# Performance work log

Measured on AMD Instinct MI355X. Metric: run time of the kernel, lower is better.

The kernel has to match this reference:

```python
import jax, jax.numpy as jnp
import numpy as np

FRAME, LATENT, HIDDEN, GATE_H, EXPERTS = 267, 32, 256, 64, 6
BATCH = 4096
IN0 = LATENT + FRAME            # 299: decoder layer-0 input (z, c)
IN1 = LATENT + HIDDEN           # 288: decoder layer-1/2 input (z, h)
OUT = FRAME                     # num_future_predictions * frame_size


def _lin(key, fan_in, fan_out):
    b = np.sqrt(1.0 / fan_in)
    return jax.random.uniform(key, (fan_in, fan_out), jnp.float32, -b, b)


def setup_inputs() -> dict:
    key = jax.random.key(0)
    ks = jax.random.split(key, 16)
    d = {
        "x": jax.random.normal(ks[0], (BATCH, FRAME), jnp.float32),
        "c": jax.random.normal(ks[1], (BATCH, FRAME), jnp.float32),
        "eps": jax.random.normal(ks[2], (BATCH, LATENT), jnp.float32),
        # encoder
        "enc_w1": _lin(ks[3], 2 * FRAME, HIDDEN), "enc_b1": jnp.zeros((HIDDEN,), jnp.float32),
        "enc_w2": _lin(ks[4], FRAME + HIDDEN, HIDDEN), "enc_b2": jnp.zeros((HIDDEN,), jnp.float32),
        "enc_wmu": _lin(ks[5], FRAME + HIDDEN, LATENT), "enc_bmu": jnp.zeros((LATENT,), jnp.float32),
        "enc_wlv": _lin(ks[6], FRAME + HIDDEN, LATENT), "enc_blv": jnp.zeros((LATENT,), jnp.float32),
        # gate MLP
        "g_w0": _lin(ks[7], IN0, GATE_H), "g_b0": jnp.zeros((GATE_H,), jnp.float32),
        "g_w1": _lin(ks[8], GATE_H, GATE_H), "g_b1": jnp.zeros((GATE_H,), jnp.float32),
        "g_w2": _lin(ks[9], GATE_H, EXPERTS), "g_b2": jnp.zeros((EXPERTS,), jnp.float32),
        # expert-mixed decoder layers (kaiming-uniform-ish init, bias 0.01)
        "w0": jax.random.uniform(ks[10], (EXPERTS, IN0, HIDDEN), jnp.float32, -np.sqrt(6.0 / IN0), np.sqrt(6.0 / IN0)),
        "b0": jnp.full((EXPERTS, HIDDEN), 0.01, jnp.float32),
        "w1": jax.random.uniform(ks[11], (EXPERTS, IN1, HIDDEN), jnp.float32, -np.sqrt(6.0 / IN1), np.sqrt(6.0 / IN1)),
        "b1": jnp.full((EXPERTS, HIDDEN), 0.01, jnp.float32),
        "w2": jax.random.uniform(ks[12], (EXPERTS, IN1, OUT), jnp.float32, -np.sqrt(6.0 / IN1), np.sqrt(6.0 / IN1)),
        "b2": jnp.full((EXPERTS, OUT), 0.01, jnp.float32),
    }
    return d


def reference(x, c, eps,
              enc_w1, enc_b1, enc_w2, enc_b2, enc_wmu, enc_bmu, enc_wlv, enc_blv,
              g_w0, g_b0, g_w1, g_b1, g_w2, g_b2,
              w0, b0, w1, b1, w2, b2):
    elu = jax.nn.elu
    # --- encoder ---
    h1 = elu(jnp.concatenate([x, c], axis=1) @ enc_w1 + enc_b1)
    h2 = elu(jnp.concatenate([x, h1], axis=1) @ enc_w2 + enc_b2)
    s = jnp.concatenate([x, h2], axis=1)
    mu = s @ enc_wmu + enc_bmu
    logvar = s @ enc_wlv + enc_blv
    z = mu + eps * jnp.exp(0.5 * logvar)
    # --- gate ---
    zc = jnp.concatenate([z, c], axis=1)
    g = elu(zc @ g_w0 + g_b0)
    g = elu(g @ g_w1 + g_b1)
    coeff = jax.nn.softmax(g @ g_w2 + g_b2, axis=1)  # [N, E]
    # --- soft-MoE decoder: blended-weight per-sample GEMMs ---
    layer = c
    for w, b, act in ((w0, b0, elu), (w1, b1, elu), (w2, b2, None)):
        inp = jnp.concatenate([z, layer], axis=1)  # [N, Din]
        # out[n,o] = sum_e coeff[n,e] * (inp[n,:] @ w[e,:,o]) + coeff[n,:] @ b[:,o]
        out = jnp.einsum('ne,ni,eio->no', coeff, inp, w) + coeff @ b
        layer = act(out) if act is not None else out
    return layer, mu, logvar
```

## Files before the change

kernel.cpp:

```cpp
#include <hip/hip_runtime.h>
#include <hip/hip_bf16.h>
#include <math.h>

#define N_BATCH 4096
#define FRAME   267
#define LATENT  32
#define HIDDEN  256
#define GATE_H  64
#define EXPERTS 6

typedef __hip_bfloat16 bf16;
typedef __bf16  bf16x8 __attribute__((ext_vector_type(8)));
typedef float   f32x4  __attribute__((ext_vector_type(4)));

__device__ __forceinline__ float eluf(float v) { return (v > 0.f) ? v : (expf(v) - 1.f); }

#define MFMA(a, b, p) __builtin_amdgcn_mfma_f32_16x16x32_bf16((a), (b), (p), 0, 0, 0)

struct WEnt { const float* src; bf16* dst; int K, M, Mtot, mOff, Ksteps, Mtiles, cum; };
struct WTab { WEnt e[10]; int total; };

__global__ __launch_bounds__(256) void prep_kernel(
    const float* __restrict__ bmu, const float* __restrict__ blv,
    float* __restrict__ biasCat, WTab tab)
{
    const int tid = threadIdx.x, bid = blockIdx.x;
    if (bid == 0 && tid < 64)
        biasCat[tid] = (tid < 32) ? bmu[tid] : blv[tid - 32];

    __shared__ float tbuf[32][33];
    int i = 0;
    while (i < 9 && bid >= tab.e[i + 1].cum) ++i;
    const WEnt en = tab.e[i];
    const int t = bid - en.cum;
    const int perE = en.Ksteps * en.Mtiles;
    const int e = t / perE;
    const int rr = t - e * perE;
    const int mt = rr / en.Ksteps;
    const int ks = rr - mt * en.Ksteps;
    const int tx = tid & 31, ty = tid >> 5;
    const float* src = en.src + (size_t)e * en.K * en.M;
    #pragma unroll
    for (int i0 = 0; i0 < 32; i0 += 8) {
        const int k = ks * 32 + i0 + ty, m = mt * 32 + tx;
        tbuf[i0 + ty][tx] = (k < en.K && m < en.M) ? src[(size_t)k * en.M + m] : 0.f;
    }
    __syncthreads();
    bf16* dst = en.dst + ((size_t)(e * en.Ksteps + ks) * en.Mtot + en.mOff + mt * 32) * 32;
    #pragma unroll
    for (int i0 = 0; i0 < 32; i0 += 8)
        dst[(size_t)(i0 + ty) * 32 + tx] = __float2bfloat16(tbuf[tx][i0 + ty]);
}

__global__ __launch_bounds__(1024, 2) void fused_kernel(
    const float* __restrict__ x, const float* __restrict__ c,
    const float* __restrict__ eps,
    const bf16* __restrict__ We1, const float* __restrict__ eb1,
    const bf16* __restrict__ We2, const float* __restrict__ eb2,
    const bf16* __restrict__ Wml, const float* __restrict__ biasCat,
    const bf16* __restrict__ Wg0, const float* __restrict__ gb0,
    const bf16* __restrict__ Wg1, const float* __restrict__ gb1,
    const bf16* __restrict__ Wg2, const float* __restrict__ gb2,
    const bf16* __restrict__ W0, const float* __restrict__ b0,
    const bf16* __restrict__ W1, const float* __restrict__ b1,
    const bf16* __restrict__ W2, const float* __restrict__ b2,
    float* __restrict__ out_layer, float* __restrict__ out_mu,
    float* __restrict__ out_lv)
{
    __shared__ bf16  bufA[16 * 552];
    __shared__ bf16  bufB[16 * 552];
    __shared__ float sML[16 * 64];
    __shared__ bf16  sG1[16 * 72];
    __shared__ bf16  sG2[16 * 72];
    __shared__ float sLg[16 * 16];
    __shared__ float sCo[EXPERTS * 16];

    const int tid  = threadIdx.x;
    const int w    = tid >> 6, lane = tid & 63, ml = lane & 15, quad = lane >> 4;
    const int row0 = blockIdx.x * 16;

    {
        const float* xr = x + (size_t)(row0 + w) * FRAME;
        const float* cr = c + (size_t)(row0 + w) * FRAME;
        #pragma unroll
        for (int j = 0; j < 9; ++j) {
            const int col = lane + j * 64;
            if (col < 544) {
                float v = 0.f;
                if (col < FRAME)          v = xr[col];
                else if (col < 2 * FRAME) v = cr[col - FRAME];
                bufA[w * 552 + col] = __float2bfloat16(v);
            }
        }
    }
    __syncthreads();

    {
        const int col = 16 * w + ml;
        f32x4 p = (f32x4){0,0,0,0};
        const bf16* wp = We1 + (size_t)col * 32 + quad * 8;
        #pragma unroll
        for (int ks = 0; ks < 17; ++ks) {
            const bf16x8 a = *(const bf16x8*)(bufA + ml * 552 + ks * 32 + quad * 8);
            p = MFMA(a, *(const bf16x8*)(wp + (size_t)ks * 256 * 32), p);
        }
        const float bv = eb1[col];
        #pragma unroll
        for (int rg = 0; rg < 4; ++rg)
            bufB[(quad * 4 + rg) * 552 + 267 + col] = __float2bfloat16(eluf(p[rg] + bv));
        #pragma unroll
        for (int j = 0; j < 5; ++j) {
            const int cc = lane + j * 64;
            if (cc < 267) bufB[w * 552 + cc] = bufA[w * 552 + cc];
        }
        if (lane < 21) bufB[w * 552 + 523 + lane] = __float2bfloat16(0.f);
    }
    __syncthreads();

    {
        const int col = 16 * w + ml;
        f32x4 p = (f32x4){0,0,0,0};
        const bf16* wp = We2 + (size_t)col * 32 + quad * 8;
        #pragma unroll
        for (int ks = 0; ks < 17; ++ks) {
            const bf16x8 a = *(const bf16x8*)(bufB + ml * 552 + ks * 32 + quad * 8);
            p = MFMA(a, *(const bf16x8*)(wp + (size_t)ks * 256 * 32), p);
        }
        __syncthreads();
        const float bv = eb2[col];
        #pragma unroll
        for (int rg = 0; rg < 4; ++rg)
            bufB[(quad * 4 + rg) * 552 + 267 + col] = __float2bfloat16(eluf(p[rg] + bv));
    }
    __syncthreads();

    if (w < 4) {
        const int col = 16 * w + ml;
        f32x4 p = (f32x4){0,0,0,0};
        const bf16* wp = Wml + (size_t)col * 32 + quad * 8;
        #pragma unroll
        for (int ks = 0; ks < 17; ++ks) {
            const bf16x8 a = *(const bf16x8*)(bufB + ml * 552 + ks * 32 + quad * 8);
            p = MFMA(a, *(const bf16x8*)(wp + (size_t)ks * 64 * 32), p);
        }
        const float bv = biasCat[col];
        #pragma unroll
        for (int rg = 0; rg < 4; ++rg)
            sML[(quad * 4 + rg) * 64 + col] = p[rg] + bv;
    }
    __syncthreads();

    if (tid < 512) {
        const int r = tid >> 5, l = tid & 31;
        const float m  = sML[r * 64 + l];
        const float lv = sML[r * 64 + 32 + l];
        const int gi = (row0 + r) * LATENT + l;
        out_mu[gi] = m; out_lv[gi] = lv;
        const bf16 zb = __float2bfloat16(m + eps[gi] * expf(0.5f * lv));
        bufA[r * 552 + l] = zb;
        bufB[r * 552 + l] = zb;
        #pragma unroll
        for (int j = 0; j < 9; ++j) {
            const int col = 32 + l + j * 32;
            bf16 v = __float2bfloat16(0.f);
            if (col < 299) v = bufA[r * 552 + 267 + (col - 32)];
            bufB[r * 552 + col] = v;
        }
    }
    __syncthreads();

    {
        const int col = 16 * w + ml;
        bf16x8 av[10];
        #pragma unroll
        for (int ks = 0; ks < 10; ++ks)
            av[ks] = *(const bf16x8*)(bufB + ml * 552 + ks * 32 + quad * 8);

        auto moe_part = [&](int e, f32x4& p) {
            const bf16* wp = W0 + ((size_t)e * 10 * 256 + col) * 32 + quad * 8;
            #pragma unroll
            for (int ks = 0; ks < 10; ++ks)
                p = MFMA(av[ks], *(const bf16x8*)(wp + (size_t)ks * 256 * 32), p);
        };

        f32x4 pe0 = (f32x4){0,0,0,0}, pe1 = (f32x4){0,0,0,0}, pe2 = (f32x4){0,0,0,0};
        f32x4 pe3 = (f32x4){0,0,0,0}, pe4 = (f32x4){0,0,0,0}, pe5 = (f32x4){0,0,0,0};

        if (w < 4) {
            f32x4 p = (f32x4){0,0,0,0};
            const bf16* wp = Wg0 + (size_t)col * 32 + quad * 8;
            #pragma unroll
            for (int ks = 0; ks < 10; ++ks)
                p = MFMA(av[ks], *(const bf16x8*)(wp + (size_t)ks * 64 * 32), p);
            const float bv = gb0[col];
            #pragma unroll
            for (int rg = 0; rg < 4; ++rg)
                sG1[(quad * 4 + rg) * 72 + col] = __float2bfloat16(eluf(p[rg] + bv));
        }
        moe_part(0, pe0); moe_part(1, pe1);
        __syncthreads();

        if (w < 4) {
            f32x4 p = (f32x4){0,0,0,0};
            const bf16* wp = Wg1 + (size_t)col * 32 + quad * 8;
            #pragma unroll
            for (int ks = 0; ks < 2; ++ks)
                p = MFMA(*(const bf16x8*)(sG1 + ml * 72 + ks * 32 + quad * 8),
                         *(const bf16x8*)(wp + (size_t)ks * 64 * 32), p);
            const float bv = gb1[col];
            #pragma unroll
            for (int rg = 0; rg < 4; ++rg)
                sG2[(quad * 4 + rg) * 72 + col] = __float2bfloat16(eluf(p[rg] + bv));
        }
        moe_part(2, pe2); moe_part(3, pe3);
        __syncthreads();

        if (w == 0) {
            f32x4 p = (f32x4){0,0,0,0};
            const bf16* wp = Wg2 + (size_t)ml * 32 + quad * 8;
            #pragma unroll
            for (int ks = 0; ks < 2; ++ks)
                p = MFMA(*(const bf16x8*)(sG2 + ml * 72 + ks * 32 + quad * 8),
                         *(const bf16x8*)(wp + (size_t)ks * 32 * 32), p);
            const float bv = (ml < EXPERTS) ? gb2[ml] : 0.f;
            #pragma unroll
            for (int rg = 0; rg < 4; ++rg)
                sLg[(quad * 4 + rg) * 16 + ml] = p[rg] + bv;
        }
        moe_part(4, pe4);
        __syncthreads();

        if (tid < 16) {
            float v[EXPERTS];
            float m = -1e30f;
            #pragma unroll
            for (int i = 0; i < EXPERTS; ++i) { v[i] = sLg[tid * 16 + i]; m = fmaxf(m, v[i]); }
            float s = 0.f;
            #pragma unroll
            for (int i = 0; i < EXPERTS; ++i) { v[i] = expf(v[i] - m); s += v[i]; }
            const float inv = 1.f / s;
            #pragma unroll
            for (int i = 0; i < EXPERTS; ++i) sCo[i * 16 + tid] = v[i] * inv;
        }
        moe_part(5, pe5);
        __syncthreads();

        f32x4 acc = (f32x4){0,0,0,0};
        auto blend = [&](const f32x4& p, int e) {
            const float bv = b0[e * 256 + col];
            #pragma unroll
            for (int rg = 0; rg < 4; ++rg)
                acc[rg] += sCo[e * 16 + quad * 4 + rg] * (p[rg] + bv);
        };
        blend(pe0, 0); blend(pe1, 1); blend(pe2, 2);
        blend(pe3, 3); blend(pe4, 4); blend(pe5, 5);
        #pragma unroll
        for (int rg = 0; rg < 4; ++rg)
            bufA[(quad * 4 + rg) * 552 + 32 + col] = __float2bfloat16(eluf(acc[rg]));
    }
    __syncthreads();

    {
        const int col = 16 * w + ml;
        bf16x8 av[9];
        #pragma unroll
        for (int ks = 0; ks < 9; ++ks)
            av[ks] = *(const bf16x8*)(bufA + ml * 552 + ks * 32 + quad * 8);
        f32x4 acc = (f32x4){0,0,0,0};
        #pragma unroll
        for (int e = 0; e < EXPERTS; ++e) {
            f32x4 p = (f32x4){0,0,0,0};
            const bf16* wp = W1 + ((size_t)e * 9 * 256 + col) * 32 + quad * 8;
            #pragma unroll
            for (int ks = 0; ks < 9; ++ks)
                p = MFMA(av[ks], *(const bf16x8*)(wp + (size_t)ks * 256 * 32), p);
            const float bv = b1[e * 256 + col];
            #pragma unroll
            for (int rg = 0; rg < 4; ++rg)
                acc[rg] += sCo[e * 16 + quad * 4 + rg] * (p[rg] + bv);
        }
        #pragma unroll
        for (int rg = 0; rg < 4; ++rg)
            bufB[(quad * 4 + rg) * 552 + 32 + col] = __float2bfloat16(eluf(acc[rg]));
    }
    __syncthreads();

    {
        bf16x8 av[9];
        #pragma unroll
        for (int ks = 0; ks < 9; ++ks)
            av[ks] = *(const bf16x8*)(bufB + ml * 552 + ks * 32 + quad * 8);
        for (int t = w; t < 18; t += 16) {
            const int col = 16 * t + ml;
            f32x4 acc = (f32x4){0,0,0,0};
            #pragma unroll
            for (int e = 0; e < EXPERTS; ++e) {
                f32x4 p = (f32x4){0,0,0,0};
                const bf16* wp = W2 + ((size_t)e * 9 * 320 + col) * 32 + quad * 8;
                #pragma unroll
                for (int ks = 0; ks < 9; ++ks)
                    p = MFMA(av[ks], *(const bf16x8*)(wp + (size_t)ks * 320 * 32), p);
                const float bv = (col < FRAME) ? b2[e * FRAME + col] : 0.f;
                #pragma unroll
                for (int rg = 0; rg < 4; ++rg)
                    acc[rg] += sCo[e * 16 + quad * 4 + rg] * (p[rg] + bv);
            }
            if (col < FRAME) {
                #pragma unroll
                for (int rg = 0; rg < 4; ++rg)
                    out_layer[(size_t)(row0 + quad * 4 + rg) * FRAME + col] = acc[rg];
            }
        }
    }
}

extern "C" void kernel_launch(void* const* d_in, const int* in_sizes, int n_in,
                              void* d_out, int out_size, void* d_ws, size_t ws_size,
                              hipStream_t stream) {
    const float* x       = (const float*)d_in[0];
    const float* c       = (const float*)d_in[1];
    const float* eps     = (const float*)d_in[2];
    const float* enc_w1  = (const float*)d_in[3];
    const float* enc_b1  = (const float*)d_in[4];
    const float* enc_w2  = (const float*)d_in[5];
    const float* enc_b2  = (const float*)d_in[6];
    const float* enc_wmu = (const float*)d_in[7];
    const float* enc_bmu = (const float*)d_in[8];
    const float* enc_wlv = (const float*)d_in[9];
    const float* enc_blv = (const float*)d_in[10];
    const float* g_w0    = (const float*)d_in[11];
    const float* g_b0    = (const float*)d_in[12];
    const float* g_w1    = (const float*)d_in[13];
    const float* g_b1    = (const float*)d_in[14];
    const float* g_w2    = (const float*)d_in[15];
    const float* g_b2    = (const float*)d_in[16];
    const float* w0      = (const float*)d_in[17];
    const float* b0      = (const float*)d_in[18];
    const float* w1      = (const float*)d_in[19];
    const float* b1      = (const float*)d_in[20];
    const float* w2      = (const float*)d_in[21];
    const float* b2      = (const float*)d_in[22];

    float* out_layer = (float*)d_out;
    float* out_mu    = out_layer + (size_t)N_BATCH * FRAME;
    float* out_lv    = out_mu    + (size_t)N_BATCH * LATENT;

    char* p = (char*)d_ws;
    float* biasCat = (float*)p;  p += 64 * 4;
    bf16* Wt_e1 = (bf16*)p;      p += (size_t)17 * 256 * 32 * 2;
    bf16* Wt_e2 = (bf16*)p;      p += (size_t)17 * 256 * 32 * 2;
    bf16* Wt_ml = (bf16*)p;      p += (size_t)17 * 64 * 32 * 2;
    bf16* Wt_g0 = (bf16*)p;      p += (size_t)10 * 64 * 32 * 2;
    bf16* Wt_g1 = (bf16*)p;      p += (size_t)2 * 64 * 32 * 2;
    bf16* Wt_g2 = (bf16*)p;      p += (size_t)2 * 32 * 32 * 2;
    bf16* Wt_w0 = (bf16*)p;      p += (size_t)EXPERTS * 10 * 256 * 32 * 2;
    bf16* Wt_w1 = (bf16*)p;      p += (size_t)EXPERTS * 9 * 256 * 32 * 2;
    bf16* Wt_w2 = (bf16*)p;      p += (size_t)EXPERTS * 9 * 320 * 32 * 2;

    WTab tab;
    int cum = 0, n = 0;
    auto add = [&](const float* src, bf16* dst, int K, int M, int Mtot, int mOff, int E) {
        int Ksteps;
        if (K == 534 || K == 523) Ksteps = 17;
        else if (K == 299) Ksteps = 10;
        else if (K == 288) Ksteps = 9;
        else Ksteps = 2;
        const int Mtiles = (M + 31) / 32;
        tab.e[n] = {src, dst, K, M, Mtot, mOff, Ksteps, Mtiles, cum};
        cum += E * Ksteps * Mtiles;
        ++n;
    };
    add(enc_w1,  Wt_e1, 534, 256, 256, 0, 1);
    add(enc_w2,  Wt_e2, 523, 256, 256, 0, 1);
    add(enc_wmu, Wt_ml, 523, 32, 64, 0, 1);
    add(enc_wlv, Wt_ml, 523, 32, 64, 32, 1);
    add(g_w0,    Wt_g0, 299, 64, 64, 0, 1);
    add(g_w1,    Wt_g1, 64, 64, 64, 0, 1);
    add(g_w2,    Wt_g2, 64, 6, 32, 0, 1);
    add(w0,      Wt_w0, 299, 256, 256, 0, EXPERTS);
    add(w1,      Wt_w1, 288, 256, 256, 0, EXPERTS);
    add(w2,      Wt_w2, 288, 267, 320, 0, EXPERTS);
    tab.total = cum;

    prep_kernel<<<dim3(cum), dim3(256), 0, stream>>>(enc_bmu, enc_blv, biasCat, tab);

    fused_kernel<<<dim3(N_BATCH / 16), dim3(1024), 0, stream>>>(
        x, c, eps,
        Wt_e1, enc_b1, Wt_e2, enc_b2, Wt_ml, biasCat,
        Wt_g0, g_b0, Wt_g1, g_b1, Wt_g2, g_b2,
        Wt_w0, b0, Wt_w1, b1, Wt_w2, b2,
        out_layer, out_mu, out_lv);
}
```

Baseline: 171.8 us.

## Split MFMA accumulator chains, move gate MLP to one wave, raise occupancy

Each MFMA reduction loop now alternates between two accumulators and sums them at the end, which breaks the serial dependency chain so consecutive MFMAs can overlap. The gate MLP (layers 0-2 plus softmax) now runs entirely in wave 0, which drops the interleaved __syncthreads that previously separated the per-expert MoE layer-0 passes. Launch bounds are raised from 2 to 4 blocks per CU, which pushes the compiler to cap registers and may cause spills. The extra accumulators also add register pressure, and the serialized gate work in wave 0 can delay the sync before the blend.

```diff
diff --git a/kernel.cpp b/kernel.cpp
--- a/kernel.cpp
+++ b/kernel.cpp
@@ -52,7 +52,7 @@
         dst[(size_t)(i0 + ty) * 32 + tx] = __float2bfloat16(tbuf[tx][i0 + ty]);
 }
 
-__global__ __launch_bounds__(1024, 2) void fused_kernel(
+__global__ __launch_bounds__(1024, 4) void fused_kernel(
     const float* __restrict__ x, const float* __restrict__ c,
     const float* __restrict__ eps,
     const bf16* __restrict__ We1, const float* __restrict__ eb1,
@@ -97,17 +97,24 @@
 
     {
         const int col = 16 * w + ml;
-        f32x4 p = (f32x4){0,0,0,0};
+        f32x4 pa = (f32x4){0,0,0,0}, pb = (f32x4){0,0,0,0};
         const bf16* wp = We1 + (size_t)col * 32 + quad * 8;
         #pragma unroll
-        for (int ks = 0; ks < 17; ++ks) {
-            const bf16x8 a = *(const bf16x8*)(bufA + ml * 552 + ks * 32 + quad * 8);
-            p = MFMA(a, *(const bf16x8*)(wp + (size_t)ks * 256 * 32), p);
+        for (int ks = 0; ks < 16; ks += 2) {
+            const bf16x8 a0 = *(const bf16x8*)(bufA + ml * 552 + ks * 32 + quad * 8);
+            const bf16x8 a1 = *(const bf16x8*)(bufA + ml * 552 + (ks + 1) * 32 + quad * 8);
+            pa = MFMA(a0, *(const bf16x8*)(wp + (size_t)ks * 256 * 32), pa);
+            pb = MFMA(a1, *(const bf16x8*)(wp + (size_t)(ks + 1) * 256 * 32), pb);
+        }
+        {
+            const bf16x8 a16 = *(const bf16x8*)(bufA + ml * 552 + 16 * 32 + quad * 8);
+            pa = MFMA(a16, *(const bf16x8*)(wp + (size_t)16 * 256 * 32), pa);
         }
         const float bv = eb1[col];
         #pragma unroll
         for (int rg = 0; rg < 4; ++rg)
-            bufB[(quad * 4 + rg) * 552 + 267 + col] = __float2bfloat16(eluf(p[rg] + bv));
+            bufB[(quad * 4 + rg) * 552 + 267 + col] =
+                __float2bfloat16(eluf(pa[rg] + pb[rg] + bv));
         #pragma unroll
         for (int j = 0; j < 5; ++j) {
             const int cc = lane + j * 64;
@@ -119,34 +126,47 @@
 
     {
         const int col = 16 * w + ml;
-        f32x4 p = (f32x4){0,0,0,0};
+        f32x4 pa = (f32x4){0,0,0,0}, pb = (f32x4){0,0,0,0};
         const bf16* wp = We2 + (size_t)col * 32 + quad * 8;
         #pragma unroll
-        for (int ks = 0; ks < 17; ++ks) {
-            const bf16x8 a = *(const bf16x8*)(bufB + ml * 552 + ks * 32 + quad * 8);
-            p = MFMA(a, *(const bf16x8*)(wp + (size_t)ks * 256 * 32), p);
+        for (int ks = 0; ks < 16; ks += 2) {
+            const bf16x8 a0 = *(const bf16x8*)(bufB + ml * 552 + ks * 32 + quad * 8);
+            const bf16x8 a1 = *(const bf16x8*)(bufB + ml * 552 + (ks + 1) * 32 + quad * 8);
+            pa = MFMA(a0, *(const bf16x8*)(wp + (size_t)ks * 256 * 32), pa);
+            pb = MFMA(a1, *(const bf16x8*)(wp + (size_t)(ks + 1) * 256 * 32), pb);
+        }
+        {
+            const bf16x8 a16 = *(const bf16x8*)(bufB + ml * 552 + 16 * 32 + quad * 8);
+            pa = MFMA(a16, *(const bf16x8*)(wp + (size_t)16 * 256 * 32), pa);
         }
         __syncthreads();
         const float bv = eb2[col];
         #pragma unroll
         for (int rg = 0; rg < 4; ++rg)
-            bufB[(quad * 4 + rg) * 552 + 267 + col] = __float2bfloat16(eluf(p[rg] + bv));
+            bufB[(quad * 4 + rg) * 552 + 267 + col] =
+                __float2bfloat16(eluf(pa[rg] + pb[rg] + bv));
     }
     __syncthreads();
 
     if (w < 4) {
         const int col = 16 * w + ml;
-        f32x4 p = (f32x4){0,0,0,0};
+        f32x4 pa = (f32x4){0,0,0,0}, pb = (f32x4){0,0,0,0};
         const bf16* wp = Wml + (size_t)col * 32 + quad * 8;
         #pragma unroll
-        for (int ks = 0; ks < 17; ++ks) {
-            const bf16x8 a = *(const bf16x8*)(bufB + ml * 552 + ks * 32 + quad * 8);
-            p = MFMA(a, *(const bf16x8*)(wp + (size_t)ks * 64 * 32), p);
+        for (int ks = 0; ks < 16; ks += 2) {
+            const bf16x8 a0 = *(const bf16x8*)(bufB + ml * 552 + ks * 32 + quad * 8);
+            const bf16x8 a1 = *(const bf16x8*)(bufB + ml * 552 + (ks + 1) * 32 + quad * 8);
+            pa = MFMA(a0, *(const bf16x8*)(wp + (size_t)ks * 64 * 32), pa);
+            pb = MFMA(a1, *(const bf16x8*)(wp + (size_t)(ks + 1) * 64 * 32), pb);
+        }
+        {
+            const bf16x8 a16 = *(const bf16x8*)(bufB + ml * 552 + 16 * 32 + quad * 8);
+            pa = MFMA(a16, *(const bf16x8*)(wp + (size_t)16 * 64 * 32), pa);
         }
         const float bv = biasCat[col];
         #pragma unroll
         for (int rg = 0; rg < 4; ++rg)
-            sML[(quad * 4 + rg) * 64 + col] = p[rg] + bv;
+            sML[(quad * 4 + rg) * 64 + col] = pa[rg] + pb[rg] + bv;
     }
     __syncthreads();
 
@@ -176,73 +196,73 @@
         for (int ks = 0; ks < 10; ++ks)
             av[ks] = *(const bf16x8*)(bufB + ml * 552 + ks * 32 + quad * 8);
 
-        auto moe_part = [&](int e, f32x4& p) {
+        if (w == 0) {
+            #pragma unroll
+            for (int t = 0; t < 4; ++t) {
+                const int gc = 16 * t + ml;
+                f32x4 p = (f32x4){0,0,0,0};
+                const bf16* wp = Wg0 + (size_t)gc * 32 + quad * 8;
+                #pragma unroll
+                for (int ks = 0; ks < 10; ++ks)
+                    p = MFMA(av[ks], *(const bf16x8*)(wp + (size_t)ks * 64 * 32), p);
+                const float bv = gb0[gc];
+                #pragma unroll
+                for (int rg = 0; rg < 4; ++rg)
+                    sG1[(quad * 4 + rg) * 72 + gc] = __float2bfloat16(eluf(p[rg] + bv));
+            }
+            #pragma unroll
+            for (int t = 0; t < 4; ++t) {
+                const int gc = 16 * t + ml;
+                f32x4 p = (f32x4){0,0,0,0};
+                const bf16* wp = Wg1 + (size_t)gc * 32 + quad * 8;
+                #pragma unroll
+                for (int ks = 0; ks < 2; ++ks)
+                    p = MFMA(*(const bf16x8*)(sG1 + ml * 72 + ks * 32 + quad * 8),
+                             *(const bf16x8*)(wp + (size_t)ks * 64 * 32), p);
+                const float bv = gb1[gc];
+                #pragma unroll
+                for (int rg = 0; rg < 4; ++rg)
+                    sG2[(quad * 4 + rg) * 72 + gc] = __float2bfloat16(eluf(p[rg] + bv));
+            }
+            {
+                f32x4 p = (f32x4){0,0,0,0};
+                const bf16* wp = Wg2 + (size_t)ml * 32 + quad * 8;
+                #pragma unroll
+                for (int ks = 0; ks < 2; ++ks)
+                    p = MFMA(*(const bf16x8*)(sG2 + ml * 72 + ks * 32 + quad * 8),
+                             *(const bf16x8*)(wp + (size_t)ks * 32 * 32), p);
+                const float bv = (ml < EXPERTS) ? gb2[ml] : 0.f;
+                #pragma unroll
+                for (int rg = 0; rg < 4; ++rg)
+                    sLg[(quad * 4 + rg) * 16 + ml] = p[rg] + bv;
+            }
+            if (lane < 16) {
+                float v[EXPERTS];
+                float m = -1e30f;
+                #pragma unroll
+                for (int i = 0; i < EXPERTS; ++i) { v[i] = sLg[lane * 16 + i]; m = fmaxf(m, v[i]); }
+                float s = 0.f;
+                #pragma unroll
+                for (int i = 0; i < EXPERTS; ++i) { v[i] = expf(v[i] - m); s += v[i]; }
+                const float inv = 1.f / s;
+                #pragma unroll
+                for (int i = 0; i < EXPERTS; ++i) sCo[i * 16 + lane] = v[i] * inv;
+            }
+        }
+
+        f32x4 pe0, pe1, pe2, pe3, pe4, pe5;
+        auto moe_part = [&](int e, f32x4& pe) {
             const bf16* wp = W0 + ((size_t)e * 10 * 256 + col) * 32 + quad * 8;
-            #pragma unroll
-            for (int ks = 0; ks < 10; ++ks)
-                p = MFMA(av[ks], *(const bf16x8*)(wp + (size_t)ks * 256 * 32), p);
+            f32x4 pa = (f32x4){0,0,0,0}, pb = (f32x4){0,0,0,0};
+            #pragma unroll
+            for (int ks = 0; ks < 10; ks += 2) {
+                pa = MFMA(av[ks],     *(const bf16x8*)(wp + (size_t)ks * 256 * 32), pa);
+                pb = MFMA(av[ks + 1], *(const bf16x8*)(wp + (size_t)(ks + 1) * 256 * 32), pb);
+            }
+            pe = pa + pb;
         };
-
-        f32x4 pe0 = (f32x4){0,0,0,0}, pe1 = (f32x4){0,0,0,0}, pe2 = (f32x4){0,0,0,0};
-        f32x4 pe3 = (f32x4){0,0,0,0}, pe4 = (f32x4){0,0,0,0}, pe5 = (f32x4){0,0,0,0};
-
-        if (w < 4) {
-            f32x4 p = (f32x4){0,0,0,0};
-            const bf16* wp = Wg0 + (size_t)col * 32 + quad * 8;
-            #pragma unroll
-            for (int ks = 0; ks < 10; ++ks)
-                p = MFMA(av[ks], *(const bf16x8*)(wp + (size_t)ks * 64 * 32), p);
-            const float bv = gb0[col];
-            #pragma unroll
-            for (int rg = 0; rg < 4; ++rg)
-                sG1[(quad * 4 + rg) * 72 + col] = __float2bfloat16(eluf(p[rg] + bv));
-        }
-        moe_part(0, pe0); moe_part(1, pe1);
-        __syncthreads();
-
-        if (w < 4) {
-            f32x4 p = (f32x4){0,0,0,0};
-            const bf16* wp = Wg1 + (size_t)col * 32 + quad * 8;
-            #pragma unroll
-            for (int ks = 0; ks < 2; ++ks)
-                p = MFMA(*(const bf16x8*)(sG1 + ml * 72 + ks * 32 + quad * 8),
-                         *(const bf16x8*)(wp + (size_t)ks * 64 * 32), p);
-            const float bv = gb1[col];
-            #pragma unroll
-            for (int rg = 0; rg < 4; ++rg)
-                sG2[(quad * 4 + rg) * 72 + col] = __float2bfloat16(eluf(p[rg] + bv));
-        }
-        moe_part(2, pe2); moe_part(3, pe3);
-        __syncthreads();
-
-        if (w == 0) {
-            f32x4 p = (f32x4){0,0,0,0};
-            const bf16* wp = Wg2 + (size_t)ml * 32 + quad * 8;
-            #pragma unroll
-            for (int ks = 0; ks < 2; ++ks)
-                p = MFMA(*(const bf16x8*)(sG2 + ml * 72 + ks * 32 + quad * 8),
-                         *(const bf16x8*)(wp + (size_t)ks * 32 * 32), p);
-            const float bv = (ml < EXPERTS) ? gb2[ml] : 0.f;
-            #pragma unroll
-            for (int rg = 0; rg < 4; ++rg)
-                sLg[(quad * 4 + rg) * 16 + ml] = p[rg] + bv;
-        }
-        moe_part(4, pe4);
-        __syncthreads();
-
-        if (tid < 16) {
-            float v[EXPERTS];
-            float m = -1e30f;
-            #pragma unroll
-            for (int i = 0; i < EXPERTS; ++i) { v[i] = sLg[tid * 16 + i]; m = fmaxf(m, v[i]); }
-            float s = 0.f;
-            #pragma unroll
-            for (int i = 0; i < EXPERTS; ++i) { v[i] = expf(v[i] - m); s += v[i]; }
-            const float inv = 1.f / s;
-            #pragma unroll
-            for (int i = 0; i < EXPERTS; ++i) sCo[i * 16 + tid] = v[i] * inv;
-        }
-        moe_part(5, pe5);
+        moe_part(0, pe0); moe_part(1, pe1); moe_part(2, pe2);
+        moe_part(3, pe3); moe_part(4, pe4); moe_part(5, pe5);
         __syncthreads();
 
         f32x4 acc = (f32x4){0,0,0,0};
@@ -269,15 +289,18 @@
         f32x4 acc = (f32x4){0,0,0,0};
         #pragma unroll
         for (int e = 0; e < EXPERTS; ++e) {
-            f32x4 p = (f32x4){0,0,0,0};
             const bf16* wp = W1 + ((size_t)e * 9 * 256 + col) * 32 + quad * 8;
-            #pragma unroll
-            for (int ks = 0; ks < 9; ++ks)
-                p = MFMA(av[ks], *(const bf16x8*)(wp + (size_t)ks * 256 * 32), p);
+            f32x4 pa = (f32x4){0,0,0,0}, pb = (f32x4){0,0,0,0};
+            #pragma unroll
+            for (int ks = 0; ks < 8; ks += 2) {
+                pa = MFMA(av[ks],     *(const bf16x8*)(wp + (size_t)ks * 256 * 32), pa);
+                pb = MFMA(av[ks + 1], *(const bf16x8*)(wp + (size_t)(ks + 1) * 256 * 32), pb);
+            }
+            pa = MFMA(av[8], *(const bf16x8*)(wp + (size_t)8 * 256 * 32), pa);
             const float bv = b1[e * 256 + col];
             #pragma unroll
             for (int rg = 0; rg < 4; ++rg)
-                acc[rg] += sCo[e * 16 + quad * 4 + rg] * (p[rg] + bv);
+                acc[rg] += sCo[e * 16 + quad * 4 + rg] * (pa[rg] + pb[rg] + bv);
         }
         #pragma unroll
         for (int rg = 0; rg < 4; ++rg)
@@ -295,15 +318,18 @@
             f32x4 acc = (f32x4){0,0,0,0};
             #pragma unroll
             for (int e = 0; e < EXPERTS; ++e) {
-                f32x4 p = (f32x4){0,0,0,0};
                 const bf16* wp = W2 + ((size_t)e * 9 * 320 + col) * 32 + quad * 8;
-                #pragma unroll
-                for (int ks = 0; ks < 9; ++ks)
-                    p = MFMA(av[ks], *(const bf16x8*)(wp + (size_t)ks * 320 * 32), p);
+                f32x4 pa = (f32x4){0,0,0,0}, pb = (f32x4){0,0,0,0};
+                #pragma unroll
+                for (int ks = 0; ks < 8; ks += 2) {
+                    pa = MFMA(av[ks],     *(const bf16x8*)(wp + (size_t)ks * 320 * 32), pa);
+                    pb = MFMA(av[ks + 1], *(const bf16x8*)(wp + (size_t)(ks + 1) * 320 * 32), pb);
+                }
+                pa = MFMA(av[8], *(const bf16x8*)(wp + (size_t)8 * 320 * 32), pa);
                 const float bv = (col < FRAME) ? b2[e * FRAME + col] : 0.f;
                 #pragma unroll
                 for (int rg = 0; rg < 4; ++rg)
-                    acc[rg] += sCo[e * 16 + quad * 4 + rg] * (p[rg] + bv);
+                    acc[rg] += sCo[e * 16 + quad * 4 + rg] * (pa[rg] + pb[rg] + bv);
             }
             if (col < FRAME) {
                 #pragma unroll
```

New measurement: 178.0 us. 1.04x slower.

## Process 32 rows per block so each weight fragment feeds two MFMAs

Applied to the files above, without the earlier changes.

Each block now handles 32 batch rows instead of 16. Every weight fragment loaded from global memory feeds two MFMAs, one per 16-row half, which halves weight traffic per row and halves the grid size. The gate MLP no longer overlaps with the expert GEMMs; it now runs as separate phases before layer 0. The mu/logvar GEMM is split over K across two warp groups whose partial sums are added afterwards. Launch bounds ask for 4 waves per SIMD, which may cause register spills. With 128 blocks the GPU may be underfilled, and the gate phases leave most warps idle.

```diff
diff --git a/kernel.cpp b/kernel.cpp
--- a/kernel.cpp
+++ b/kernel.cpp
@@ -52,7 +52,7 @@
         dst[(size_t)(i0 + ty) * 32 + tx] = __float2bfloat16(tbuf[tx][i0 + ty]);
 }
 
-__global__ __launch_bounds__(1024, 2) void fused_kernel(
+__global__ __launch_bounds__(1024, 4) void fused_kernel(
     const float* __restrict__ x, const float* __restrict__ c,
     const float* __restrict__ eps,
     const bf16* __restrict__ We1, const float* __restrict__ eb1,
@@ -67,93 +67,107 @@
     float* __restrict__ out_layer, float* __restrict__ out_mu,
     float* __restrict__ out_lv)
 {
-    __shared__ bf16  bufA[16 * 552];
-    __shared__ bf16  bufB[16 * 552];
-    __shared__ float sML[16 * 64];
-    __shared__ bf16  sG1[16 * 72];
-    __shared__ bf16  sG2[16 * 72];
-    __shared__ float sLg[16 * 16];
-    __shared__ float sCo[EXPERTS * 16];
+    __shared__ bf16  bufA[32 * 552];
+    __shared__ bf16  bufB[32 * 552];
+    __shared__ float sMLp[2][32 * 64];
+    __shared__ bf16  sG1[32 * 72];
+    __shared__ bf16  sG2[32 * 72];
+    __shared__ float sLg[32 * 16];
+    __shared__ float sCo[EXPERTS * 32];
 
     const int tid  = threadIdx.x;
     const int w    = tid >> 6, lane = tid & 63, ml = lane & 15, quad = lane >> 4;
-    const int row0 = blockIdx.x * 16;
-
-    {
-        const float* xr = x + (size_t)(row0 + w) * FRAME;
-        const float* cr = c + (size_t)(row0 + w) * FRAME;
-        #pragma unroll
-        for (int j = 0; j < 9; ++j) {
-            const int col = lane + j * 64;
-            if (col < 544) {
-                float v = 0.f;
-                if (col < FRAME)          v = xr[col];
-                else if (col < 2 * FRAME) v = cr[col - FRAME];
-                bufA[w * 552 + col] = __float2bfloat16(v);
-            }
-        }
-    }
-    __syncthreads();
-
-    {
-        const int col = 16 * w + ml;
-        f32x4 p = (f32x4){0,0,0,0};
-        const bf16* wp = We1 + (size_t)col * 32 + quad * 8;
+    const int row0 = blockIdx.x * 32;
+
+    {
+        #pragma unroll
+        for (int rr = 0; rr < 2; ++rr) {
+            const int r = w + rr * 16;
+            const float* xr = x + (size_t)(row0 + r) * FRAME;
+            const float* cr = c + (size_t)(row0 + r) * FRAME;
+            #pragma unroll
+            for (int j = 0; j < 9; ++j) {
+                const int col = lane + j * 64;
+                if (col < 544) {
+                    float v = 0.f;
+                    if (col < FRAME)          v = xr[col];
+                    else if (col < 2 * FRAME) v = cr[col - FRAME];
+                    bufA[r * 552 + col] = __float2bfloat16(v);
+                }
+            }
+        }
+    }
+    __syncthreads();
+
+    {
+        const int col = 16 * w + ml;
+        const bf16* wq = We1 + (size_t)col * 32 + quad * 8;
+        f32x4 a0 = (f32x4){0,0,0,0}, a1 = (f32x4){0,0,0,0};
         #pragma unroll
         for (int ks = 0; ks < 17; ++ks) {
-            const bf16x8 a = *(const bf16x8*)(bufA + ml * 552 + ks * 32 + quad * 8);
-            p = MFMA(a, *(const bf16x8*)(wp + (size_t)ks * 256 * 32), p);
+            const bf16x8 b = *(const bf16x8*)(wq + (size_t)ks * 8192);
+            a0 = MFMA(*(const bf16x8*)(bufA + ml * 552 + ks * 32 + quad * 8), b, a0);
+            a1 = MFMA(*(const bf16x8*)(bufA + (16 + ml) * 552 + ks * 32 + quad * 8), b, a1);
         }
         const float bv = eb1[col];
         #pragma unroll
-        for (int rg = 0; rg < 4; ++rg)
-            bufB[(quad * 4 + rg) * 552 + 267 + col] = __float2bfloat16(eluf(p[rg] + bv));
-        #pragma unroll
-        for (int j = 0; j < 5; ++j) {
-            const int cc = lane + j * 64;
-            if (cc < 267) bufB[w * 552 + cc] = bufA[w * 552 + cc];
-        }
-        if (lane < 21) bufB[w * 552 + 523 + lane] = __float2bfloat16(0.f);
-    }
-    __syncthreads();
-
-    {
-        const int col = 16 * w + ml;
-        f32x4 p = (f32x4){0,0,0,0};
-        const bf16* wp = We2 + (size_t)col * 32 + quad * 8;
+        for (int rg = 0; rg < 4; ++rg) {
+            bufB[(quad * 4 + rg) * 552 + 267 + col]      = __float2bfloat16(eluf(a0[rg] + bv));
+            bufB[(16 + quad * 4 + rg) * 552 + 267 + col] = __float2bfloat16(eluf(a1[rg] + bv));
+        }
+        #pragma unroll
+        for (int rr = 0; rr < 2; ++rr) {
+            const int r = w + rr * 16;
+            #pragma unroll
+            for (int j = 0; j < 5; ++j) {
+                const int cc = lane + j * 64;
+                if (cc < 267) bufB[r * 552 + cc] = bufA[r * 552 + cc];
+            }
+            if (lane < 21) bufB[r * 552 + 523 + lane] = __float2bfloat16(0.f);
+        }
+    }
+    __syncthreads();
+
+    {
+        const int col = 16 * w + ml;
+        const bf16* wq = We2 + (size_t)col * 32 + quad * 8;
+        f32x4 a0 = (f32x4){0,0,0,0}, a1 = (f32x4){0,0,0,0};
         #pragma unroll
         for (int ks = 0; ks < 17; ++ks) {
-            const bf16x8 a = *(const bf16x8*)(bufB + ml * 552 + ks * 32 + quad * 8);
-            p = MFMA(a, *(const bf16x8*)(wp + (size_t)ks * 256 * 32), p);
+            const bf16x8 b = *(const bf16x8*)(wq + (size_t)ks * 8192);
+            a0 = MFMA(*(const bf16x8*)(bufB + ml * 552 + ks * 32 + quad * 8), b, a0);
+            a1 = MFMA(*(const bf16x8*)(bufB + (16 + ml) * 552 + ks * 32 + quad * 8), b, a1);
         }
         __syncthreads();
         const float bv = eb2[col];
         #pragma unroll
-        for (int rg = 0; rg < 4; ++rg)
-            bufB[(quad * 4 + rg) * 552 + 267 + col] = __float2bfloat16(eluf(p[rg] + bv));
-    }
-    __syncthreads();
-
-    if (w < 4) {
-        const int col = 16 * w + ml;
+        for (int rg = 0; rg < 4; ++rg) {
+            bufB[(quad * 4 + rg) * 552 + 267 + col]      = __float2bfloat16(eluf(a0[rg] + bv));
+            bufB[(16 + quad * 4 + rg) * 552 + 267 + col] = __float2bfloat16(eluf(a1[rg] + bv));
+        }
+    }
+    __syncthreads();
+
+    {
+        const int ct = w & 3, rg = (w >> 2) & 1, kg = w >> 3;
+        const int col = 16 * ct + ml;
+        const int rbase = rg * 16;
+        const int k0 = kg ? 9 : 0, k1 = kg ? 17 : 9;
+        const bf16* wq = Wml + (size_t)col * 32 + quad * 8;
         f32x4 p = (f32x4){0,0,0,0};
-        const bf16* wp = Wml + (size_t)col * 32 + quad * 8;
-        #pragma unroll
-        for (int ks = 0; ks < 17; ++ks) {
-            const bf16x8 a = *(const bf16x8*)(bufB + ml * 552 + ks * 32 + quad * 8);
-            p = MFMA(a, *(const bf16x8*)(wp + (size_t)ks * 64 * 32), p);
-        }
-        const float bv = biasCat[col];
-        #pragma unroll
-        for (int rg = 0; rg < 4; ++rg)
-            sML[(quad * 4 + rg) * 64 + col] = p[rg] + bv;
-    }
-    __syncthreads();
-
-    if (tid < 512) {
+        for (int ks = k0; ks < k1; ++ks)
+            p = MFMA(*(const bf16x8*)(bufB + (rbase + ml) * 552 + ks * 32 + quad * 8),
+                     *(const bf16x8*)(wq + (size_t)ks * 2048), p);
+        #pragma unroll
+        for (int rg2 = 0; rg2 < 4; ++rg2)
+            sMLp[kg][(rbase + quad * 4 + rg2) * 64 + col] = p[rg2];
+    }
+    __syncthreads();
+
+    {
         const int r = tid >> 5, l = tid & 31;
-        const float m  = sML[r * 64 + l];
-        const float lv = sML[r * 64 + 32 + l];
+        const float m  = sMLp[0][r * 64 + l] + sMLp[1][r * 64 + l] + biasCat[l];
+        const float lv = sMLp[0][r * 64 + 32 + l] + sMLp[1][r * 64 + 32 + l] + biasCat[32 + l];
         const int gi = (row0 + r) * LATENT + l;
         out_mu[gi] = m; out_lv[gi] = lv;
         const bf16 zb = __float2bfloat16(m + eps[gi] * expf(0.5f * lv));
@@ -169,146 +183,156 @@
     }
     __syncthreads();
 
-    {
-        const int col = 16 * w + ml;
-        bf16x8 av[10];
-        #pragma unroll
-        for (int ks = 0; ks < 10; ++ks)
-            av[ks] = *(const bf16x8*)(bufB + ml * 552 + ks * 32 + quad * 8);
-
-        auto moe_part = [&](int e, f32x4& p) {
-            const bf16* wp = W0 + ((size_t)e * 10 * 256 + col) * 32 + quad * 8;
-            #pragma unroll
-            for (int ks = 0; ks < 10; ++ks)
-                p = MFMA(av[ks], *(const bf16x8*)(wp + (size_t)ks * 256 * 32), p);
-        };
-
-        f32x4 pe0 = (f32x4){0,0,0,0}, pe1 = (f32x4){0,0,0,0}, pe2 = (f32x4){0,0,0,0};
-        f32x4 pe3 = (f32x4){0,0,0,0}, pe4 = (f32x4){0,0,0,0}, pe5 = (f32x4){0,0,0,0};
-
-        if (w < 4) {
-            f32x4 p = (f32x4){0,0,0,0};
-            const bf16* wp = Wg0 + (size_t)col * 32 + quad * 8;
-            #pragma unroll
-            for (int ks = 0; ks < 10; ++ks)
-                p = MFMA(av[ks], *(const bf16x8*)(wp + (size_t)ks * 64 * 32), p);
-            const float bv = gb0[col];
-            #pragma unroll
-            for (int rg = 0; rg < 4; ++rg)
-                sG1[(quad * 4 + rg) * 72 + col] = __float2bfloat16(eluf(p[rg] + bv));
-        }
-        moe_part(0, pe0); moe_part(1, pe1);
-        __syncthreads();
-
-        if (w < 4) {
-            f32x4 p = (f32x4){0,0,0,0};
-            const bf16* wp = Wg1 + (size_t)col * 32 + quad * 8;
-            #pragma unroll
-            for (int ks = 0; ks < 2; ++ks)
-                p = MFMA(*(const bf16x8*)(sG1 + ml * 72 + ks * 32 + quad * 8),
-                         *(const bf16x8*)(wp + (size_t)ks * 64 * 32), p);
-            const float bv = gb1[col];
-            #pragma unroll
-            for (int rg = 0; rg < 4; ++rg)
-                sG2[(quad * 4 + rg) * 72 + col] = __float2bfloat16(eluf(p[rg] + bv));
-        }
-        moe_part(2, pe2); moe_part(3, pe3);
-        __syncthreads();
-
-        if (w == 0) {
-            f32x4 p = (f32x4){0,0,0,0};
-            const bf16* wp = Wg2 + (size_t)ml * 32 + quad * 8;
-            #pragma unroll
-            for (int ks = 0; ks < 2; ++ks)
-                p = MFMA(*(const bf16x8*)(sG2 + ml * 72 + ks * 32 + quad * 8),
-                         *(const bf16x8*)(wp + (size_t)ks * 32 * 32), p);
-            const float bv = (ml < EXPERTS) ? gb2[ml] : 0.f;
-            #pragma unroll
-            for (int rg = 0; rg < 4; ++rg)
-                sLg[(quad * 4 + rg) * 16 + ml] = p[rg] + bv;
-        }
-        moe_part(4, pe4);
-        __syncthreads();
-
-        if (tid < 16) {
-            float v[EXPERTS];
-            float m = -1e30f;
-            #pragma unroll
-            for (int i = 0; i < EXPERTS; ++i) { v[i] = sLg[tid * 16 + i]; m = fmaxf(m, v[i]); }
-            float s = 0.f;
-            #pragma unroll
-            for (int i = 0; i < EXPERTS; ++i) { v[i] = expf(v[i] - m); s += v[i]; }
-            const float inv = 1.f / s;
-            #pragma unroll
-            for (int i = 0; i < EXPERTS; ++i) sCo[i * 16 + tid] = v[i] * inv;
-        }
-        moe_part(5, pe5);
-        __syncthreads();
-
-        f32x4 acc = (f32x4){0,0,0,0};
-        auto blend = [&](const f32x4& p, int e) {
+    if (w < 4) {
+        const int col = 16 * w + ml;
+        const bf16* gq = Wg0 + (size_t)col * 32 + quad * 8;
+        f32x4 p0 = (f32x4){0,0,0,0}, p1 = (f32x4){0,0,0,0};
+        #pragma unroll
+        for (int ks = 0; ks < 10; ++ks) {
+            const bf16x8 b = *(const bf16x8*)(gq + (size_t)ks * 2048);
+            p0 = MFMA(*(const bf16x8*)(bufB + ml * 552 + ks * 32 + quad * 8), b, p0);
+            p1 = MFMA(*(const bf16x8*)(bufB + (16 + ml) * 552 + ks * 32 + quad * 8), b, p1);
+        }
+        const float bv = gb0[col];
+        #pragma unroll
+        for (int rg = 0; rg < 4; ++rg) {
+            sG1[(quad * 4 + rg) * 72 + col]      = __float2bfloat16(eluf(p0[rg] + bv));
+            sG1[(16 + quad * 4 + rg) * 72 + col] = __float2bfloat16(eluf(p1[rg] + bv));
+        }
+    }
+    __syncthreads();
+    if (w < 4) {
+        const int col = 16 * w + ml;
+        const bf16* gq = Wg1 + (size_t)col * 32 + quad * 8;
+        f32x4 p0 = (f32x4){0,0,0,0}, p1 = (f32x4){0,0,0,0};
+        #pragma unroll
+        for (int ks = 0; ks < 2; ++ks) {
+            const bf16x8 b = *(const bf16x8*)(gq + (size_t)ks * 2048);
+            p0 = MFMA(*(const bf16x8*)(sG1 + ml * 72 + ks * 32 + quad * 8), b, p0);
+            p1 = MFMA(*(const bf16x8*)(sG1 + (16 + ml) * 72 + ks * 32 + quad * 8), b, p1);
+        }
+        const float bv = gb1[col];
+        #pragma unroll
+        for (int rg = 0; rg < 4; ++rg) {
+            sG2[(quad * 4 + rg) * 72 + col]      = __float2bfloat16(eluf(p0[rg] + bv));
+            sG2[(16 + quad * 4 + rg) * 72 + col] = __float2bfloat16(eluf(p1[rg] + bv));
+        }
+    }
+    __syncthreads();
+    if (w == 0) {
+        const bf16* gq = Wg2 + (size_t)ml * 32 + quad * 8;
+        f32x4 p0 = (f32x4){0,0,0,0}, p1 = (f32x4){0,0,0,0};
+        #pragma unroll
+        for (int ks = 0; ks < 2; ++ks) {
+            const bf16x8 b = *(const bf16x8*)(gq + (size_t)ks * 1024);
+            p0 = MFMA(*(const bf16x8*)(sG2 + ml * 72 + ks * 32 + quad * 8), b, p0);
+            p1 = MFMA(*(const bf16x8*)(sG2 + (16 + ml) * 72 + ks * 32 + quad * 8), b, p1);
+        }
+        const float bv = (ml < EXPERTS) ? gb2[ml] : 0.f;
+        #pragma unroll
+        for (int rg = 0; rg < 4; ++rg) {
+            sLg[(quad * 4 + rg) * 16 + ml]      = p0[rg] + bv;
+            sLg[(16 + quad * 4 + rg) * 16 + ml] = p1[rg] + bv;
+        }
+    }
+    __syncthreads();
+    if (tid < 32) {
+        float v[EXPERTS];
+        float m = -1e30f;
+        #pragma unroll
+        for (int i = 0; i < EXPERTS; ++i) { v[i] = sLg[tid * 16 + i]; m = fmaxf(m, v[i]); }
+        float s = 0.f;
+        #pragma unroll
+        for (int i = 0; i < EXPERTS; ++i) { v[i] = expf(v[i] - m); s += v[i]; }
+        const float inv = 1.f / s;
+        #pragma unroll
+        for (int i = 0; i < EXPERTS; ++i) sCo[i * 32 + tid] = v[i] * inv;
+    }
+    __syncthreads();
+
+    {
+        const int col = 16 * w + ml;
+        const bf16* wq = W0 + (size_t)col * 32 + quad * 8;
+        f32x4 acc0 = (f32x4){0,0,0,0}, acc1 = (f32x4){0,0,0,0};
+        #pragma unroll
+        for (int e = 0; e < EXPERTS; ++e) {
+            f32x4 p0 = (f32x4){0,0,0,0}, p1 = (f32x4){0,0,0,0};
+            #pragma unroll
+            for (int ks = 0; ks < 10; ++ks) {
+                const bf16x8 b = *(const bf16x8*)(wq + (size_t)(e * 10 + ks) * 8192);
+                p0 = MFMA(*(const bf16x8*)(bufB + ml * 552 + ks * 32 + quad * 8), b, p0);
+                p1 = MFMA(*(const bf16x8*)(bufB + (16 + ml) * 552 + ks * 32 + quad * 8), b, p1);
+            }
             const float bv = b0[e * 256 + col];
             #pragma unroll
-            for (int rg = 0; rg < 4; ++rg)
-                acc[rg] += sCo[e * 16 + quad * 4 + rg] * (p[rg] + bv);
-        };
-        blend(pe0, 0); blend(pe1, 1); blend(pe2, 2);
-        blend(pe3, 3); blend(pe4, 4); blend(pe5, 5);
-        #pragma unroll
-        for (int rg = 0; rg < 4; ++rg)
-            bufA[(quad * 4 + rg) * 552 + 32 + col] = __float2bfloat16(eluf(acc[rg]));
-    }
-    __syncthreads();
-
-    {
-        const int col = 16 * w + ml;
-        bf16x8 av[9];
-        #pragma unroll
-        for (int ks = 0; ks < 9; ++ks)
-            av[ks] = *(const bf16x8*)(bufA + ml * 552 + ks * 32 + quad * 8);
-        f32x4 acc = (f32x4){0,0,0,0};
+            for (int rg = 0; rg < 4; ++rg) {
+                acc0[rg] += sCo[e * 32 + quad * 4 + rg]      * (p0[rg] + bv);
+                acc1[rg] += sCo[e * 32 + 16 + quad * 4 + rg] * (p1[rg] + bv);
+            }
+        }
+        #pragma unroll
+        for (int rg = 0; rg < 4; ++rg) {
+            bufA[(quad * 4 + rg) * 552 + 32 + col]      = __float2bfloat16(eluf(acc0[rg]));
+            bufA[(16 + quad * 4 + rg) * 552 + 32 + col] = __float2bfloat16(eluf(acc1[rg]));
+        }
+    }
+    __syncthreads();
+
+    {
+        const int col = 16 * w + ml;
+        const bf16* wq = W1 + (size_t)col * 32 + quad * 8;
+        f32x4 acc0 = (f32x4){0,0,0,0}, acc1 = (f32x4){0,0,0,0};
         #pragma unroll
         for (int e = 0; e < EXPERTS; ++e) {
-            f32x4 p = (f32x4){0,0,0,0};
-            const bf16* wp = W1 + ((size_t)e * 9 * 256 + col) * 32 + quad * 8;
-            #pragma unroll
-            for (int ks = 0; ks < 9; ++ks)
-                p = MFMA(av[ks], *(const bf16x8*)(wp + (size_t)ks * 256 * 32), p);
+            f32x4 p0 = (f32x4){0,0,0,0}, p1 = (f32x4){0,0,0,0};
+            #pragma unroll
+            for (int ks = 0; ks < 9; ++ks) {
+                const bf16x8 b = *(const bf16x8*)(wq + (size_t)(e * 9 + ks) * 8192);
+                p0 = MFMA(*(const bf16x8*)(bufA + ml * 552 + ks * 32 + quad * 8), b, p0);
+                p1 = MFMA(*(const bf16x8*)(bufA + (16 + ml) * 552 + ks * 32 + quad * 8), b, p1);
+            }
             const float bv = b1[e * 256 + col];
             #pragma unroll
-            for (int rg = 0; rg < 4; ++rg)
-                acc[rg] += sCo[e * 16 + quad * 4 + rg] * (p[rg] + bv);
-        }
-        #pragma unroll
-        for (int rg = 0; rg < 4; ++rg)
-            bufB[(quad * 4 + rg) * 552 + 32 + col] = __float2bfloat16(eluf(acc[rg]));
-    }
-    __syncthreads();
-
-    {
-        bf16x8 av[9];
-        #pragma unroll
-        for (int ks = 0; ks < 9; ++ks)
-            av[ks] = *(const bf16x8*)(bufB + ml * 552 + ks * 32 + quad * 8);
-        for (int t = w; t < 18; t += 16) {
+            for (int rg = 0; rg < 4; ++rg) {
+                acc0[rg] += sCo[e * 32 + quad * 4 + rg]      * (p0[rg] + bv);
+                acc1[rg] += sCo[e * 32 + 16 + quad * 4 + rg] * (p1[rg] + bv);
+            }
+        }
+        #pragma unroll
+        for (int rg = 0; rg < 4; ++rg) {
+            bufB[(quad * 4 + rg) * 552 + 32 + col]      = __float2bfloat16(eluf(acc0[rg]));
+            bufB[(16 + quad * 4 + rg) * 552 + 32 + col] = __float2bfloat16(eluf(acc1[rg]));
+        }
+    }
+    __syncthreads();
+
+    {
+        for (int t = w; t < 17; t += 16) {
             const int col = 16 * t + ml;
-            f32x4 acc = (f32x4){0,0,0,0};
+            const bf16* wq = W2 + (size_t)col * 32 + quad * 8;
+            f32x4 acc0 = (f32x4){0,0,0,0}, acc1 = (f32x4){0,0,0,0};
             #pragma unroll
             for (int e = 0; e < EXPERTS; ++e) {
-                f32x4 p = (f32x4){0,0,0,0};
-                const bf16* wp = W2 + ((size_t)e * 9 * 320 + col) * 32 + quad * 8;
+                f32x4 p0 = (f32x4){0,0,0,0}, p1 = (f32x4){0,0,0,0};
                 #pragma unroll
-                for (int ks = 0; ks < 9; ++ks)
-                    p = MFMA(av[ks], *(const bf16x8*)(wp + (size_t)ks * 320 * 32), p);
+                for (int ks = 0; ks < 9; ++ks) {
+                    const bf16x8 b = *(const bf16x8*)(wq + (size_t)(e * 9 + ks) * 10240);
+                    p0 = MFMA(*(const bf16x8*)(bufB + ml * 552 + ks * 32 + quad * 8), b, p0);
+                    p1 = MFMA(*(const bf16x8*)(bufB + (16 + ml) * 552 + ks * 32 + quad * 8), b, p1);
+                }
                 const float bv = (col < FRAME) ? b2[e * FRAME + col] : 0.f;
                 #pragma unroll
-                for (int rg = 0; rg < 4; ++rg)
-                    acc[rg] += sCo[e * 16 + quad * 4 + rg] * (p[rg] + bv);
+                for (int rg = 0; rg < 4; ++rg) {
+                    acc0[rg] += sCo[e * 32 + quad * 4 + rg]      * (p0[rg] + bv);
+                    acc1[rg] += sCo[e * 32 + 16 + quad * 4 + rg] * (p1[rg] + bv);
+                }
             }
             if (col < FRAME) {
                 #pragma unroll
-                for (int rg = 0; rg < 4; ++rg)
-                    out_layer[(size_t)(row0 + quad * 4 + rg) * FRAME + col] = acc[rg];
+                for (int rg = 0; rg < 4; ++rg) {
+                    out_layer[(size_t)(row0 + quad * 4 + rg) * FRAME + col]      = acc0[rg];
+                    out_layer[(size_t)(row0 + 16 + quad * 4 + rg) * FRAME + col] = acc1[rg];
+                }
             }
         }
     }
@@ -384,7 +408,7 @@
 
     prep_kernel<<<dim3(cum), dim3(256), 0, stream>>>(enc_bmu, enc_blv, biasCat, tab);
 
-    fused_kernel<<<dim3(N_BATCH / 16), dim3(1024), 0, stream>>>(
+    fused_kernel<<<dim3(N_BATCH / 32), dim3(1024), 0, stream>>>(
         x, c, eps,
         Wt_e1, enc_b1, Wt_e2, enc_b2, Wt_ml, biasCat,
         Wt_g0, g_b0, Wt_g1, g_b1, Wt_g2, g_b2,
```

New measurement: 241.4 us. 40.5% more time.
